# Kernel tuning notes

Measured on AMD Instinct MI355X. Metric: run time of the kernel, lower is better.

The kernel has to match this reference:

```python
import jax, jax.numpy as jnp
import numpy as np

MIN_SCALE = 0.05
MAX_SCALE = 0.2
EPS = 0.001
RATE = 4
SUBSAMPLE = 3


def box_filter(x, k):
    # matches torch: pad (1+p) before / p after on H and W, double cumsum + subtract
    if k % 2 == 0:
        k = k + 1
    p = k // 2
    xp = jnp.pad(x, ((0, 0), (0, 0), (1 + p, p), (1 + p, p)))
    c = jnp.cumsum(xp, axis=2)
    y = c[:, :, k:, :] - c[:, :, :-k, :]
    c2 = jnp.cumsum(y, axis=3)
    return c2[:, :, :, k:] - c2[:, :, :, :-k]


def _resize(x, h, w):
    # torch F.interpolate(mode='bilinear', align_corners=False) == jax bilinear, no antialias
    n, c = x.shape[0], x.shape[1]
    return jax.image.resize(x, (n, c, h, w), method='bilinear', antialias=False)


def rf_norm(x):
    N, C, H, W = x.shape
    scale = MAX_SCALE
    it = 1
    while True:  # loop bounds depend only on static config -> Python loop is jit-safe
        win = int(max(H, W) * scale)
        if win < 3 and it == 1:
            mean = x.mean(axis=(1, 2, 3), keepdims=True)
            std = x.std(axis=(1, 2, 3), ddof=1, keepdims=True) + EPS
            x = x / std - mean / std
        else:
            if SUBSAMPLE > 1 and min(H, W) > SUBSAMPLE * 10 and win > SUBSAMPLE * 5:
                xs = _resize(x, H // SUBSAMPLE, W // SUBSAMPLE)
                win = win // SUBSAMPLE
            else:
                xs = x
            h, w = xs.shape[2], xs.shape[3]
            ones = jnp.ones((1, 1, h, w), x.dtype)
            M = box_filter(ones, win)
            x_mean = box_filter(xs, win).mean(axis=1, keepdims=True) / M
            x2_mean = box_filter(xs ** 2, win).mean(axis=1, keepdims=True) / M
            var = jnp.clip(x2_mean - x_mean ** 2, 0.0) + EPS
            std = jnp.sqrt(var)
            a = 1.0 / std
            b = -x_mean / std
            mean_a = box_filter(a, win) / M
            mean_b = box_filter(b, win) / M
            if SUBSAMPLE > 1:
                mean_a = _resize(mean_a, H, W)
                mean_b = _resize(mean_b, H, W)
            x = mean_a * x + mean_b
        it += 1
        scale /= RATE  # coarse_to_fine=True
        if scale < MIN_SCALE:
            break
    return x


def setup_inputs() -> dict:
    key = jax.random.key(0)
    x = jax.random.normal(key, (16, 3, 768, 768), dtype=jnp.float32)
    return {"x": x}


def reference(x):
    return rf_norm(x)
```

## Files before the change

### kernel.cpp

```cpp
#include <hip/hip_runtime.h>


#define N_B 16
#define CCH 3
#define HF 768
#define HL 256
#define SLICE (HL * HL)
#define TOT_L (N_B * SLICE)
#define EPSV 1e-3f

__device__ __forceinline__ int cnt(int i, int P) {
  int hi = i + P; if (hi > HL - 1) hi = HL - 1;
  int lo = i - P; if (lo < 0) lo = 0;
  return hi - lo + 1;
}

template <int G>
__device__ __forceinline__ void scan2g(float a, float b, int g, int j,
    float2 (*s)[HL], float2 (*wt)[4]) {
  int lane = j & 63, w = j >> 6;
#pragma unroll
  for (int d = 1; d < 64; d <<= 1) {
    float ta = __shfl_up(a, (unsigned)d);
    float tb = __shfl_up(b, (unsigned)d);
    if (lane >= d) { a += ta; b += tb; }
  }
  if (lane == 63) wt[g][w] = make_float2(a, b);
  __syncthreads();
  float offa = 0.f, offb = 0.f;
  for (int ww = 0; ww < w; ++ww) { float2 t = wt[g][ww]; offa += t.x; offb += t.y; }
  s[g][j] = make_float2(a + offa, b + offb);
  __syncthreads();
}

template <int P>
__device__ __forceinline__ float2 boxr(const float2 (*s)[HL], int g, int j) {
  int hi = j + P; if (hi > HL - 1) hi = HL - 1;
  int lo = j - P - 1;
  float2 r = s[g][hi];
  if (lo >= 0) { float2 l = s[g][lo]; r.x -= l.x; r.y -= l.y; }
  return r;
}

template <int P>
__device__ __forceinline__ void xpose_store(const float2 (*s)[HL], int tid,
    float2* __restrict__ dst, size_t nb, int col0) {
  if (tid < 512) {
    int row = tid & 255, half = tid >> 8;
    float2 r0 = boxr<P>(s, 2 * half, row);
    float2 r1 = boxr<P>(s, 2 * half + 1, row);
    float4* d = (float4*)(dst + nb + (size_t)row * HL + col0);
    d[half] = make_float4(r0.x, r0.y, r1.x, r1.y);
  }
}

__global__ __launch_bounds__(1024) void k1(const float* __restrict__ x,
    float2* __restrict__ UV, float2* __restrict__ Spk) {
  __shared__ float2 sA[4][HL];
  __shared__ float2 wtA[4][4];
  int b = blockIdx.x;
  int n = b >> 6;
  int ib = (b & 63) << 2;
  int tid = threadIdx.x;
  int g = tid >> 8, j = tid & 255;
  const float* xp = x + (size_t)n * CCH * HF * HF
                  + (size_t)(3 * (ib + g) + 1) * HF + (3 * j + 1);
  float c0 = xp[0], c1 = xp[HF * HF], c2 = xp[2 * HF * HF];
  float uu = (c0 + c1 + c2) * (1.f / 3.f);
  float vv = (c0 * c0 + c1 * c1 + c2 * c2) * (1.f / 3.f);
  size_t nb = (size_t)n * SLICE;
  UV[nb + (size_t)(ib + g) * HL + j] = make_float2(uu, vv);
  scan2g<4>(uu, vv, g, j, sA, wtA);
  xpose_store<25>(sA, tid, Spk, nb, ib);
}

__global__ __launch_bounds__(1024) void k2(const float2* __restrict__ Spk,
    float2* __restrict__ Ppk) {
  __shared__ float2 sA[4][HL], sB[4][HL];
  __shared__ float2 wtA[4][4], wtB[4][4];
  int n = blockIdx.x >> 6, strip = blockIdx.x & 63;
  int tid = threadIdx.x, g = tid >> 8, j = tid & 255;
  int c = strip * 4 + g;
  size_t nb = (size_t)n * SLICE;
  float2 sv = Spk[nb + (size_t)c * HL + j];
  scan2g<4>(sv.x, sv.y, g, j, sA, wtA);
  float2 bu = boxr<25>(sA, g, j);
  float invM = 1.f / ((float)cnt(j, 25) * (float)cnt(c, 25));
  float xm = bu.x * invM, x2m = bu.y * invM;
  float var = x2m - xm * xm; if (var < 0.f) var = 0.f;
  float inv = 1.f / sqrtf(var + EPSV);
  scan2g<4>(inv, -xm * inv, g, j, sB, wtB);
  xpose_store<25>(sB, tid, Ppk, nb, strip * 4);
}

__global__ __launch_bounds__(1024) void k3(const float2* __restrict__ Ppk,
    const float2* __restrict__ UV, float2* __restrict__ AB1,
    float2* __restrict__ Qpk) {
  __shared__ float2 sA[4][HL], sB[4][HL];
  __shared__ float2 wtA[4][4], wtB[4][4];
  int n = blockIdx.x >> 6, strip = blockIdx.x & 63;
  int tid = threadIdx.x, g = tid >> 8, j = tid & 255;
  int i = strip * 4 + g;
  size_t nb = (size_t)n * SLICE;
  size_t idx = nb + (size_t)i * HL + j;
  float2 pv = Ppk[idx];
  scan2g<4>(pv.x, pv.y, g, j, sA, wtA);
  float2 bb = boxr<25>(sA, g, j);
  float invM = 1.f / ((float)cnt(i, 25) * (float)cnt(j, 25));
  float Av = bb.x * invM, Bv = bb.y * invM;
  AB1[idx] = make_float2(Av, Bv);
  float2 uv = UV[idx];
  float u2 = Av * uv.x + Bv;
  float v2 = Av * Av * uv.y + 2.f * Av * Bv * uv.x + Bv * Bv;
  scan2g<4>(u2, v2, g, j, sB, wtB);
  xpose_store<6>(sB, tid, Qpk, nb, strip * 4);
}

__global__ __launch_bounds__(1024) void k4(const float2* __restrict__ Qpk,
    float2* __restrict__ Rpk) {
  __shared__ float2 sA[4][HL], sB[4][HL];
  __shared__ float2 wtA[4][4], wtB[4][4];
  int n = blockIdx.x >> 6, strip = blockIdx.x & 63;
  int tid = threadIdx.x, g = tid >> 8, j = tid & 255;
  int c = strip * 4 + g;
  size_t nb = (size_t)n * SLICE;
  float2 qv = Qpk[nb + (size_t)c * HL + j];
  scan2g<4>(qv.x, qv.y, g, j, sA, wtA);
  float2 bu = boxr<6>(sA, g, j);
  float invM = 1.f / ((float)cnt(j, 6) * (float)cnt(c, 6));
  float xm = bu.x * invM, x2m = bu.y * invM;
  float var = x2m - xm * xm; if (var < 0.f) var = 0.f;
  float inv = 1.f / sqrtf(var + EPSV);
  scan2g<4>(inv, -xm * inv, g, j, sB, wtB);
  xpose_store<6>(sB, tid, Rpk, nb, strip * 4);
}

__device__ __forceinline__ void upw(int q, int& i0, int& i1, float& w1) {
  int d = q / 3;
  int r = q - 3 * d;
  if (r == 1) { i0 = d; i1 = d; w1 = 0.f; }
  else if (r == 2) { i0 = d; i1 = d + 1; if (i1 > HL - 1) i1 = HL - 1; w1 = 1.f / 3.f; }
  else { i1 = d; i0 = d - 1; if (i0 < 0) i0 = 0; w1 = 2.f / 3.f; }
}

__global__ __launch_bounds__(768) void k_final(
    const float* __restrict__ x, const float2* __restrict__ AB1,
    const float2* __restrict__ Rpk, float* __restrict__ out) {
  __shared__ float2 s[3][HL];
  __shared__ float2 wt[3][4];
  __shared__ float2 ry01[3][HL], ry23[3][HL];
  int nb_ = blockIdx.x;
  int d = nb_ & 255, n = nb_ >> 8;
  int tid = threadIdx.x, g = tid >> 8, j = tid & 255;
  size_t mb = (size_t)n * SLICE;
  int rg = d - 1 + g; rg = rg < 0 ? 0 : (rg > HL - 1 ? HL - 1 : rg);
  float2 rv = Rpk[mb + (size_t)rg * HL + j];
  scan2g<3>(rv.x, rv.y, g, j, s, wt);
  int s0 = (g == 0) ? 0 : 1;
  int s1 = (g == 2) ? 2 : 1;
  float wy1 = (g == 0) ? (2.f / 3.f) : ((g == 2) ? (1.f / 3.f) : 0.f);
  float wy0 = 1.f - wy1;
  int r0 = d - 1 + s0; r0 = r0 < 0 ? 0 : (r0 > HL - 1 ? HL - 1 : r0);
  int r1 = d - 1 + s1; r1 = r1 < 0 ? 0 : (r1 > HL - 1 ? HL - 1 : r1);
  float cj6 = (float)cnt(j, 6);
  float2 b0 = boxr<6>(s, s0, j);
  float2 b1 = boxr<6>(s, s1, j);
  float i0f = 1.f / ((float)cnt(r0, 6) * cj6);
  float i1f = 1.f / ((float)cnt(r1, 6) * cj6);
  ry23[g][j] = make_float2(wy0 * b0.x * i0f + wy1 * b1.x * i1f,
                           wy0 * b0.y * i0f + wy1 * b1.y * i1f);
  float2 a0 = AB1[mb + (size_t)r0 * HL + j];
  float2 a1 = AB1[mb + (size_t)r1 * HL + j];
  ry01[g][j] = make_float2(wy0 * a0.x + wy1 * a1.x, wy0 * a0.y + wy1 * a1.y);
  __syncthreads();
  if (j < 192) {
    int y = 3 * d + g;
    float A1c[4], B1c[4], A2c[4], B2c[4];
#pragma unroll
    for (int e = 0; e < 4; ++e) {
      int q = 4 * j + e;
      int ix0, ix1;
      float wx1;
      upw(q, ix0, ix1, wx1);
      float wx0 = 1.f - wx1;
      float2 m0 = ry01[g][ix0], m1 = ry01[g][ix1];
      float2 m2 = ry23[g][ix0], m3 = ry23[g][ix1];
      A1c[e] = wx0 * m0.x + wx1 * m1.x;
      B1c[e] = wx0 * m0.y + wx1 * m1.y;
      A2c[e] = wx0 * m2.x + wx1 * m3.x;
      B2c[e] = wx0 * m2.y + wx1 * m3.y;
    }
    size_t rowbase = ((size_t)(n * CCH) * HF + y) * HF + 4 * j;
#pragma unroll
    for (int c = 0; c < CCH; ++c) {
      const float4 xin = *(const float4*)(x + rowbase + (size_t)c * HF * HF);
      float4 o;
      o.x = A2c[0] * (A1c[0] * xin.x + B1c[0]) + B2c[0];
      o.y = A2c[1] * (A1c[1] * xin.y + B1c[1]) + B2c[1];
      o.z = A2c[2] * (A1c[2] * xin.z + B1c[2]) + B2c[2];
      o.w = A2c[3] * (A1c[3] * xin.w + B1c[3]) + B2c[3];
      *(float4*)(out + rowbase + (size_t)c * HF * HF) = o;
    }
  }
}

extern "C" void kernel_launch(void* const* d_in, const int* in_sizes, int n_in,
                              void* d_out, int out_size, void* d_ws, size_t ws_size,
                              hipStream_t stream) {
  const float* x = (const float*)d_in[0];
  float* out = (float*)d_out;
  const size_t S = (size_t)TOT_L;
  float2 *UV, *Spk, *Ppk, *AB1, *Rpk, *Qpk;
  if (ws_size >= 10 * S * sizeof(float)) {
    float2* w = (float2*)d_ws;
    UV = w; Spk = UV + S; Ppk = Spk + S; AB1 = Ppk + S; Rpk = AB1 + S;
  } else {
    AB1 = (float2*)d_ws; Rpk = AB1 + S;
    UV = (float2*)out; Spk = UV + S; Ppk = Spk + S;
  }
  Qpk = Spk;

  k1<<<N_B * 64, 1024, 0, stream>>>(x, UV, Spk);
  k2<<<N_B * 64, 1024, 0, stream>>>(Spk, Ppk);
  k3<<<N_B * 64, 1024, 0, stream>>>(Ppk, UV, AB1, Qpk);
  k4<<<N_B * 64, 1024, 0, stream>>>(Qpk, Rpk);
  k_final<<<N_B * HL, 768, 0, stream>>>(x, AB1, Rpk, out);
}
```

Before: 98.50 us.

## Split final box filter into separate kernel and simplify per-row final apply

The second-scale box-filter scan on Rpk moves out of k_final into a new kernel k5 that writes AB2 once per low-resolution pixel. k_final then runs one 256-thread block per output row and only does bilinear interpolation of AB1 and AB2 before the affine apply. This removes the scan work that the old k_final repeated for each set of three output rows. In exchange it adds a kernel launch and an extra 16*256*256 float2 buffer written and read through global memory, and it needs a larger workspace.

```diff
diff --git a/kernel.cpp b/kernel.cpp
--- a/kernel.cpp
+++ b/kernel.cpp
@@ -135,6 +135,22 @@
   xpose_store<6>(sB, tid, Rpk, nb, strip * 4);
 }
 
+__global__ __launch_bounds__(1024) void k5(const float2* __restrict__ Rpk,
+    float2* __restrict__ AB2) {
+  __shared__ float2 sA[4][HL];
+  __shared__ float2 wtA[4][4];
+  int n = blockIdx.x >> 6, strip = blockIdx.x & 63;
+  int tid = threadIdx.x, g = tid >> 8, j = tid & 255;
+  int i = strip * 4 + g;
+  size_t nb = (size_t)n * SLICE;
+  size_t idx = nb + (size_t)i * HL + j;
+  float2 rv = Rpk[idx];
+  scan2g<4>(rv.x, rv.y, g, j, sA, wtA);
+  float2 bb = boxr<6>(sA, g, j);
+  float invM = 1.f / ((float)cnt(i, 6) * (float)cnt(j, 6));
+  AB2[idx] = make_float2(bb.x * invM, bb.y * invM);
+}
+
 __device__ __forceinline__ void upw(int q, int& i0, int& i1, float& w1) {
   int d = q / 3;
   int r = q - 3 * d;
@@ -143,54 +159,42 @@
   else { i1 = d; i0 = d - 1; if (i0 < 0) i0 = 0; w1 = 2.f / 3.f; }
 }
 
-__global__ __launch_bounds__(768) void k_final(
+__global__ __launch_bounds__(256) void k_final(
     const float* __restrict__ x, const float2* __restrict__ AB1,
-    const float2* __restrict__ Rpk, float* __restrict__ out) {
-  __shared__ float2 s[3][HL];
-  __shared__ float2 wt[3][4];
-  __shared__ float2 ry01[3][HL], ry23[3][HL];
+    const float2* __restrict__ AB2, float* __restrict__ out) {
+  __shared__ float4 ry[HL];
   int nb_ = blockIdx.x;
-  int d = nb_ & 255, n = nb_ >> 8;
-  int tid = threadIdx.x, g = tid >> 8, j = tid & 255;
+  int y = nb_ % HF;
+  int n = nb_ / HF;
+  int t = threadIdx.x;
+  int iy0, iy1;
+  float wy1;
+  upw(y, iy0, iy1, wy1);
+  float wy0 = 1.f - wy1;
   size_t mb = (size_t)n * SLICE;
-  int rg = d - 1 + g; rg = rg < 0 ? 0 : (rg > HL - 1 ? HL - 1 : rg);
-  float2 rv = Rpk[mb + (size_t)rg * HL + j];
-  scan2g<3>(rv.x, rv.y, g, j, s, wt);
-  int s0 = (g == 0) ? 0 : 1;
-  int s1 = (g == 2) ? 2 : 1;
-  float wy1 = (g == 0) ? (2.f / 3.f) : ((g == 2) ? (1.f / 3.f) : 0.f);
-  float wy0 = 1.f - wy1;
-  int r0 = d - 1 + s0; r0 = r0 < 0 ? 0 : (r0 > HL - 1 ? HL - 1 : r0);
-  int r1 = d - 1 + s1; r1 = r1 < 0 ? 0 : (r1 > HL - 1 ? HL - 1 : r1);
-  float cj6 = (float)cnt(j, 6);
-  float2 b0 = boxr<6>(s, s0, j);
-  float2 b1 = boxr<6>(s, s1, j);
-  float i0f = 1.f / ((float)cnt(r0, 6) * cj6);
-  float i1f = 1.f / ((float)cnt(r1, 6) * cj6);
-  ry23[g][j] = make_float2(wy0 * b0.x * i0f + wy1 * b1.x * i1f,
-                           wy0 * b0.y * i0f + wy1 * b1.y * i1f);
-  float2 a0 = AB1[mb + (size_t)r0 * HL + j];
-  float2 a1 = AB1[mb + (size_t)r1 * HL + j];
-  ry01[g][j] = make_float2(wy0 * a0.x + wy1 * a1.x, wy0 * a0.y + wy1 * a1.y);
+  float2 a0 = AB1[mb + (size_t)iy0 * HL + t];
+  float2 a1 = AB1[mb + (size_t)iy1 * HL + t];
+  float2 c0v = AB2[mb + (size_t)iy0 * HL + t];
+  float2 c1v = AB2[mb + (size_t)iy1 * HL + t];
+  ry[t] = make_float4(wy0 * a0.x + wy1 * a1.x, wy0 * a0.y + wy1 * a1.y,
+                      wy0 * c0v.x + wy1 * c1v.x, wy0 * c0v.y + wy1 * c1v.y);
   __syncthreads();
-  if (j < 192) {
-    int y = 3 * d + g;
+  if (t < 192) {
     float A1c[4], B1c[4], A2c[4], B2c[4];
 #pragma unroll
     for (int e = 0; e < 4; ++e) {
-      int q = 4 * j + e;
+      int q = 4 * t + e;
       int ix0, ix1;
       float wx1;
       upw(q, ix0, ix1, wx1);
       float wx0 = 1.f - wx1;
-      float2 m0 = ry01[g][ix0], m1 = ry01[g][ix1];
-      float2 m2 = ry23[g][ix0], m3 = ry23[g][ix1];
+      float4 m0 = ry[ix0], m1 = ry[ix1];
       A1c[e] = wx0 * m0.x + wx1 * m1.x;
       B1c[e] = wx0 * m0.y + wx1 * m1.y;
-      A2c[e] = wx0 * m2.x + wx1 * m3.x;
-      B2c[e] = wx0 * m2.y + wx1 * m3.y;
+      A2c[e] = wx0 * m0.z + wx1 * m1.z;
+      B2c[e] = wx0 * m0.w + wx1 * m1.w;
     }
-    size_t rowbase = ((size_t)(n * CCH) * HF + y) * HF + 4 * j;
+    size_t rowbase = ((size_t)(n * CCH) * HF + y) * HF + 4 * t;
 #pragma unroll
     for (int c = 0; c < CCH; ++c) {
       const float4 xin = *(const float4*)(x + rowbase + (size_t)c * HF * HF);
@@ -210,13 +214,14 @@
   const float* x = (const float*)d_in[0];
   float* out = (float*)d_out;
   const size_t S = (size_t)TOT_L;
-  float2 *UV, *Spk, *Ppk, *AB1, *Rpk, *Qpk;
-  if (ws_size >= 10 * S * sizeof(float)) {
+  float2 *UV, *Spk, *Ppk, *AB1, *Rpk, *AB2, *Qpk;
+  if (ws_size >= 12 * S * sizeof(float)) {
     float2* w = (float2*)d_ws;
     UV = w; Spk = UV + S; Ppk = Spk + S; AB1 = Ppk + S; Rpk = AB1 + S;
+    AB2 = Rpk + S;
   } else {
-    AB1 = (float2*)d_ws; Rpk = AB1 + S;
-    UV = (float2*)out; Spk = UV + S; Ppk = Spk + S;
+    AB1 = (float2*)d_ws; AB2 = AB1 + S;
+    UV = (float2*)out; Spk = UV + S; Ppk = Spk + S; Rpk = Ppk + S;
   }
   Qpk = Spk;
 
@@ -224,5 +229,6 @@
   k2<<<N_B * 64, 1024, 0, stream>>>(Spk, Ppk);
   k3<<<N_B * 64, 1024, 0, stream>>>(Ppk, UV, AB1, Qpk);
   k4<<<N_B * 64, 1024, 0, stream>>>(Qpk, Rpk);
-  k_final<<<N_B * HL, 768, 0, stream>>>(x, AB1, Rpk, out);
-}
+  k5<<<N_B * 64, 1024, 0, stream>>>(Rpk, AB2);
+  k_final<<<N_B * HF, 256, 0, stream>>>(x, AB1, AB2, out);
+}
```

Result: slower. 102.2 us (+3.8%).
